# Kernel optimization log

Measured on AMD Instinct MI355X. Metric: run time of the kernel, lower is better.

Reference implementation:

```python
import jax, jax.numpy as jnp
import numpy as np

# --- constants from HodgkinHuxleyODE defaults ---
G_LEAK = 0.1
GBAR_NA = 4.0
GBAR_K = 1.5
GBAR_M = 0.07
C_MEM = 1.0
E_NA = 53.0
E_K = -107.0
E_LEAK = -70.0
VT = -60.0
TAU_MAX = 600.0
I_ON = 0.0
I_OFF = np.inf
CURR_LEVEL = 0.0005
A_SOMA = 3.141592653589793 * (70.0 * 1e-4) ** 2

B = 8388608  # batch size


def efun(z):
    # z/(exp(z)-1), with Taylor expansion 1 - z/2 near z=0 (|z| < 1e-4)
    small = jnp.abs(z) < 1e-4
    zs = jnp.where(small, 1.0, z)  # safe value to avoid 0/0 (and NaN grads)
    return jnp.where(small, 1.0 - z / 2.0, zs / (jnp.exp(zs) - 1.0))


def alpha_m(x):
    return 0.32 * efun(-0.25 * (x - VT - 13.0)) / 0.25

def beta_m(x):
    return 0.28 * efun(0.2 * (x - VT - 40.0)) / 0.2

def alpha_h(x):
    return 0.128 * jnp.exp(-(x - VT - 17.0) / 18.0)

def beta_h(x):
    return 4.0 / (1.0 + jnp.exp(-0.2 * (x - VT - 40.0)))

def alpha_n(x):
    return 0.032 * efun(-0.2 * (x - VT - 15.0)) / 0.2

def beta_n(x):
    return 0.5 * jnp.exp(-(x - VT - 10.0) / 40.0)

def p_inf(x):
    return 1.0 / (1.0 + jnp.exp(-0.1 * (x + 35.0)))

def tau_p(x):
    v1 = x + 35.0
    return TAU_MAX / (3.3 * jnp.exp(0.05 * v1) + jnp.exp(-0.05 * v1))


def setup_inputs() -> dict:
    key = jax.random.key(0)
    kV, kn, km, kh, kp = jax.random.split(key, 5)
    return {
        "t": 1,
        "V": jax.random.normal(kV, (B, 1), dtype=jnp.float32),
        "n": jax.random.uniform(kn, (B, 1), dtype=jnp.float32),
        "m": jax.random.uniform(km, (B, 1), dtype=jnp.float32),
        "h": jax.random.uniform(kh, (B, 1), dtype=jnp.float32),
        "p": jax.random.uniform(kp, (B, 1), dtype=jnp.float32),
    }


def reference(t, V, n, m, h, p):
    # input current (t is a static Python scalar)
    I_in = (CURR_LEVEL / A_SOMA) if (t > I_ON and t < I_OFF) else 0.0

    a_n, b_n = alpha_n(V), beta_n(V)
    a_m, b_m = alpha_m(V), beta_m(V)
    a_h, b_h = alpha_h(V), beta_h(V)

    dV = (m ** 3 * GBAR_NA * h * (E_NA - V)
          + n ** 4 * GBAR_K * (E_K - V)
          + GBAR_M * p * (E_K - V)
          + G_LEAK * (E_LEAK - V)
          + I_in)
    dV = C_MEM * dV

    # dx = (x_inf - x) / tau_x = alpha - (alpha + beta) * x
    dn = (a_n / (a_n + b_n) - n) * (a_n + b_n)
    dm = (a_m / (a_m + b_m) - m) * (a_m + b_m)
    dh = (a_h / (a_h + b_h) - h) * (a_h + b_h)
    dp = (p_inf(V) - p) / tau_p(V)
    return (dV, dn, dm, dh, dp)
```

## Files before the change

### kernel.cpp

```cpp
#include <hip/hip_runtime.h>
#include <math.h>

namespace {

typedef float f32x4 __attribute__((ext_vector_type(4)));

__device__ __forceinline__ float rcp_f(float x) { return __builtin_amdgcn_rcpf(x); }

__device__ __forceinline__ float efun(float z) {
    float e = __expf(z);
    float big = z * rcp_f(e - 1.0f);
    float small = 1.0f - 0.5f * z;
    return (fabsf(z) < 1e-4f) ? small : big;
}

struct F5 { float dV, dn, dm, dh, dp; };

__device__ __forceinline__ F5 hh(float V, float n, float m, float h, float p, float I_in) {
    float a_n = 0.16f  * efun(-0.2f  * (V + 45.0f));
    float a_m = 1.28f  * efun(-0.25f * (V + 47.0f));
    float b_n = 0.5f   * __expf((V + 50.0f) * -0.025f);
    float a_h = 0.128f * __expf((V + 43.0f) * (-1.0f / 18.0f));

    float zb = 0.2f * (V + 20.0f);
    float eb = __expf(zb);
    float bm_big = zb * rcp_f(eb - 1.0f);
    float b_m = 1.4f * ((fabsf(zb) < 1e-4f) ? (1.0f - 0.5f * zb) : bm_big);
    float b_h = 4.0f - 4.0f * rcp_f(eb + 1.0f);

    float ekv = -107.0f - V;
    float m3  = m * m * m;
    float n2  = n * n;

    F5 r;
    r.dV = 4.0f  * m3 * h * (53.0f - V)
         + 1.5f  * (n2 * n2) * ekv
         + 0.07f * p * ekv
         + 0.1f  * (-70.0f - V)
         + I_in;

    float sn = a_n + b_n; r.dn = a_n - sn * n;
    float sm = a_m + b_m; r.dm = a_m - sm * m;
    float sh = a_h + b_h; r.dh = a_h - sh * h;

    float v1   = V + 35.0f;
    float e5   = __expf(0.05f * v1);
    float re5  = rcp_f(e5);
    float pinf = rcp_f(1.0f + re5 * re5);
    float itau = (3.3f * e5 + re5) * (1.0f / 600.0f);
    r.dp = (pinf - p) * itau;
    return r;
}

__device__ __forceinline__ void hh4(f32x4 V, f32x4 n, f32x4 m, f32x4 h, f32x4 p,
                                    float I_in, f32x4 o[5]) {
    F5 a = hh(V.x, n.x, m.x, h.x, p.x, I_in);
    F5 b = hh(V.y, n.y, m.y, h.y, p.y, I_in);
    F5 c = hh(V.z, n.z, m.z, h.z, p.z, I_in);
    F5 d = hh(V.w, n.w, m.w, h.w, p.w, I_in);
    o[0].x = a.dV; o[0].y = b.dV; o[0].z = c.dV; o[0].w = d.dV;
    o[1].x = a.dn; o[1].y = b.dn; o[1].z = c.dn; o[1].w = d.dn;
    o[2].x = a.dm; o[2].y = b.dm; o[2].z = c.dm; o[2].w = d.dm;
    o[3].x = a.dh; o[3].y = b.dh; o[3].z = c.dh; o[3].w = d.dh;
    o[4].x = a.dp; o[4].y = b.dp; o[4].z = c.dp; o[4].w = d.dp;
}

__global__ __launch_bounds__(256) void hh_kernel(
    const int* __restrict__ tptr,
    const f32x4* __restrict__ V4, const f32x4* __restrict__ n4,
    const f32x4* __restrict__ m4, const f32x4* __restrict__ h4,
    const f32x4* __restrict__ p4,
    f32x4* __restrict__ out4, int nb8, int nb4, float i_in_level)
{
    int i = blockIdx.x * blockDim.x + threadIdx.x;
    if (i >= nb8) return;
    int j = i + nb8;

    float t = (float)(*tptr);
    float I_in = (t > 0.0f) ? i_in_level : 0.0f;

    f32x4 V0 = V4[i], n0 = n4[i], m0 = m4[i], h0 = h4[i], p0 = p4[i];
    f32x4 V1 = V4[j], n1 = n4[j], m1 = m4[j], h1 = h4[j], p1 = p4[j];

    f32x4 o[5];
    hh4(V0, n0, m0, h0, p0, I_in, o);
    out4[i          ] = o[0];
    out4[i +     nb4] = o[1];
    out4[i + 2 * nb4] = o[2];
    out4[i + 3 * nb4] = o[3];
    out4[i + 4 * nb4] = o[4];

    hh4(V1, n1, m1, h1, p1, I_in, o);
    out4[j          ] = o[0];
    out4[j +     nb4] = o[1];
    out4[j + 2 * nb4] = o[2];
    out4[j + 3 * nb4] = o[3];
    out4[j + 4 * nb4] = o[4];
}

}

extern "C" void kernel_launch(void* const* d_in, const int* in_sizes, int n_in,
                              void* d_out, int out_size, void* d_ws, size_t ws_size,
                              hipStream_t stream) {
    const int*   t = (const int*)  d_in[0];
    const f32x4* V = (const f32x4*)d_in[1];
    const f32x4* n = (const f32x4*)d_in[2];
    const f32x4* m = (const f32x4*)d_in[3];
    const f32x4* h = (const f32x4*)d_in[4];
    const f32x4* p = (const f32x4*)d_in[5];

    int B   = in_sizes[1];
    int nb4 = B / 4;
    int nb8 = nb4 / 2;

    float i_in = (float)(0.0005 / (3.141592653589793 * 70.0e-4 * 70.0e-4));

    int block = 256;
    int grid  = (nb8 + block - 1) / block;
    hh_kernel<<<grid, block, 0, stream>>>(t, V, n, m, h, p, (f32x4*)d_out, nb8, nb4, i_in);
}
```

Baseline: 298.0 us.

## Software-pipeline loads across a grid-stride loop of four iterations per thread

Each thread now handles four float4 groups spaced a grid-wide stride apart instead of two adjacent halves. The loads for the next group are issued before the current group is computed and stored, with sched_barriers pinning that order, so memory latency overlaps the exp-heavy math. The grid shrinks by half, which lowers occupancy, and it relies on the compiler honouring the barrier placement.

```diff
diff --git a/kernel.cpp b/kernel.cpp
--- a/kernel.cpp
+++ b/kernel.cpp
@@ -65,37 +65,48 @@
     o[4].x = a.dp; o[4].y = b.dp; o[4].z = c.dp; o[4].w = d.dp;
 }
 
+constexpr int NITER = 4;
+
 __global__ __launch_bounds__(256) void hh_kernel(
     const int* __restrict__ tptr,
     const f32x4* __restrict__ V4, const f32x4* __restrict__ n4,
     const f32x4* __restrict__ m4, const f32x4* __restrict__ h4,
     const f32x4* __restrict__ p4,
-    f32x4* __restrict__ out4, int nb8, int nb4, float i_in_level)
+    f32x4* __restrict__ out4, int nb4, int stride, float i_in_level)
 {
     int i = blockIdx.x * blockDim.x + threadIdx.x;
-    if (i >= nb8) return;
-    int j = i + nb8;
 
     float t = (float)(*tptr);
     float I_in = (t > 0.0f) ? i_in_level : 0.0f;
 
-    f32x4 V0 = V4[i], n0 = n4[i], m0 = m4[i], h0 = h4[i], p0 = p4[i];
-    f32x4 V1 = V4[j], n1 = n4[j], m1 = m4[j], h1 = h4[j], p1 = p4[j];
+    f32x4 V0, n0, m0, h0, p0;
+    if (i < nb4) {
+        V0 = V4[i]; n0 = n4[i]; m0 = m4[i]; h0 = h4[i]; p0 = p4[i];
+    }
+    __builtin_amdgcn_sched_barrier(0);
 
-    f32x4 o[5];
-    hh4(V0, n0, m0, h0, p0, I_in, o);
-    out4[i          ] = o[0];
-    out4[i +     nb4] = o[1];
-    out4[i + 2 * nb4] = o[2];
-    out4[i + 3 * nb4] = o[3];
-    out4[i + 4 * nb4] = o[4];
+#pragma unroll
+    for (int k = 0; k < NITER; ++k) {
+        int inext = i + stride;
+        f32x4 V1, n1, m1, h1, p1;
+        if (k + 1 < NITER && inext < nb4) {
+            V1 = V4[inext]; n1 = n4[inext]; m1 = m4[inext]; h1 = h4[inext]; p1 = p4[inext];
+        }
+        __builtin_amdgcn_sched_barrier(0);
 
-    hh4(V1, n1, m1, h1, p1, I_in, o);
-    out4[j          ] = o[0];
-    out4[j +     nb4] = o[1];
-    out4[j + 2 * nb4] = o[2];
-    out4[j + 3 * nb4] = o[3];
-    out4[j + 4 * nb4] = o[4];
+        if (i < nb4) {
+            f32x4 o[5];
+            hh4(V0, n0, m0, h0, p0, I_in, o);
+            out4[i          ] = o[0];
+            out4[i +     nb4] = o[1];
+            out4[i + 2 * nb4] = o[2];
+            out4[i + 3 * nb4] = o[3];
+            out4[i + 4 * nb4] = o[4];
+        }
+
+        V0 = V1; n0 = n1; m0 = m1; h0 = h1; p0 = p1;
+        i = inext;
+    }
 }
 
 }
@@ -112,11 +123,13 @@
 
     int B   = in_sizes[1];
     int nb4 = B / 4;
-    int nb8 = nb4 / 2;
 
     float i_in = (float)(0.0005 / (3.141592653589793 * 70.0e-4 * 70.0e-4));
 
-    int block = 256;
-    int grid  = (nb8 + block - 1) / block;
-    hh_kernel<<<grid, block, 0, stream>>>(t, V, n, m, h, p, (f32x4*)d_out, nb8, nb4, i_in);
+    int block    = 256;
+    int nthreads = (nb4 + NITER - 1) / NITER;
+    int grid     = (nthreads + block - 1) / block;
+    int stride   = grid * block;
+
+    hh_kernel<<<grid, block, 0, stream>>>(t, V, n, m, h, p, (f32x4*)d_out, nb4, stride, i_in);
 }
```

Measured after the change: 298.3 us. About the same (+0.1%).
